# Optimization experiments

Measured on AMD Instinct MI355X. Metric: run time of the kernel, lower is better.

The kernel has to match this reference:

```python
import jax, jax.numpy as jnp
import numpy as np

B, S, D, H, HD = 4, 2048, 768, 12, 64
P = H * HD
LR = 0.1

def _ln(x, g, b, eps=1e-5):
    m = jnp.mean(x, axis=-1, keepdims=True)
    v = jnp.mean((x - m) ** 2, axis=-1, keepdims=True)
    return (x - m) / jnp.sqrt(v + eps) * g + b

def _modifier(x, w1, b1, w2, b2):
    # Linear -> GELU(exact) -> Linear, matching nn.Sequential(Linear, GELU, Linear)
    h = jax.nn.gelu(x @ w1.T + b1, approximate=False)
    return h @ w2.T + b2

def setup_inputs() -> dict:
    key = jax.random.key(0)
    ks = jax.random.split(key, 16)
    def n(k, shape, s=0.02):
        return jax.random.normal(k, shape, jnp.float32) * s
    inp = {}
    inp['x'] = jax.random.normal(ks[0], (B, S, D), jnp.float32)
    inp['ln_in_g'] = jnp.ones((D,), jnp.float32)
    inp['ln_in_b'] = jnp.zeros((D,), jnp.float32)
    inp['Wk'] = n(ks[1], (P, D))
    inp['Wv'] = n(ks[2], (P, D))
    inp['Wq'] = n(ks[3], (P, D))
    inp['km_w1'] = n(ks[4], (D // 4, D), 0.01); inp['km_b1'] = jnp.zeros((D // 4,), jnp.float32)
    inp['km_w2'] = n(ks[5], (P, D // 4), 0.01); inp['km_b2'] = jnp.zeros((P,), jnp.float32)
    inp['vm_w1'] = n(ks[6], (D // 4, D), 0.01); inp['vm_b1'] = jnp.zeros((D // 4,), jnp.float32)
    inp['vm_w2'] = n(ks[7], (P, D // 4), 0.01); inp['vm_b2'] = jnp.zeros((P,), jnp.float32)
    inp['qm_w1'] = n(ks[8], (D // 4, D), 0.01); inp['qm_b1'] = jnp.zeros((D // 4,), jnp.float32)
    inp['qm_w2'] = n(ks[9], (P, D // 4), 0.01); inp['qm_b2'] = jnp.zeros((P,), jnp.float32)
    inp['lnk_g'] = jnp.ones((HD,), jnp.float32); inp['lnk_b'] = jnp.zeros((HD,), jnp.float32)
    inp['lnv_g'] = jnp.ones((HD,), jnp.float32); inp['lnv_b'] = jnp.zeros((HD,), jnp.float32)
    inp['lnq_g'] = jnp.ones((HD,), jnp.float32); inp['lnq_b'] = jnp.zeros((HD,), jnp.float32)
    inp['Wo'] = n(ks[10], (D, P))
    inp['lr_scale'] = jnp.ones((H,), jnp.float32)
    inp['Wg'] = n(ks[11], (D, D))
    inp['bg'] = jnp.zeros((D,), jnp.float32)
    return inp

def reference(x, ln_in_g, ln_in_b, Wk, Wv, Wq,
              km_w1, km_b1, km_w2, km_b2,
              vm_w1, vm_b1, vm_w2, vm_b2,
              qm_w1, qm_b1, qm_w2, qm_b2,
              lnk_g, lnk_b, lnv_g, lnv_b, lnq_g, lnq_b,
              Wo, lr_scale, Wg, bg):
    b, s, d = x.shape
    xn = _ln(x, ln_in_g, ln_in_b)  # norm_input
    # data-dependent projections (context defaults to x_normed)
    k = xn @ Wk.T + 0.1 * _modifier(xn, km_w1, km_b1, km_w2, km_b2)
    v = xn @ Wv.T + 0.1 * _modifier(xn, vm_w1, vm_b1, vm_w2, vm_b2)
    q = xn @ Wq.T + 0.1 * _modifier(xn, qm_w1, qm_b1, qm_w2, qm_b2)
    k = _ln(k.reshape(b, s, H, HD), lnk_g, lnk_b)
    v = _ln(v.reshape(b, s, H, HD), lnv_g, lnv_b)
    q = _ln(q.reshape(b, s, H, HD), lnq_g, lnq_b)
    # scan over time: (s, b, h, d)
    k_s = jnp.transpose(k, (1, 0, 2, 3))
    v_s = jnp.transpose(v, (1, 0, 2, 3))
    q_s = jnp.transpose(q, (1, 0, 2, 3))
    lr = jax.nn.sigmoid(lr_scale) * LR * 2.0  # (H,)
    M0 = jnp.zeros((b, H, HD, HD), x.dtype)

    def step(M, kvq):
        k_t, v_t, q_t = kvq  # each (b, h, d)
        out_t = jnp.einsum('bhdk,bhk->bhd', M, q_t)  # read before update
        kn = k_t / (jnp.linalg.norm(k_t, axis=-1, keepdims=True) + 1e-6)
        pred = jnp.einsum('bhdk,bhk->bhd', M, kn)
        surprise = pred - v_t
        # M - outer(pred, kn) - lr * outer(surprise, kn), fused
        coef = pred + lr[None, :, None] * surprise  # (b, h, d)
        M_new = M - jnp.einsum('bhd,bhk->bhdk', coef, kn)
        return M_new, out_t

    M_final, outs = jax.lax.scan(step, M0, (k_s, v_s, q_s))  # outs: (s, b, h, d)
    out = jnp.transpose(outs, (1, 0, 2, 3)).reshape(b, s, H * HD)
    out = out @ Wo.T
    gate = jax.nn.sigmoid(x @ Wg.T + bg)  # output_gate on raw x
    out = gate * out
    return out, M_final
```

## Files before the change

### kernel.cpp

```cpp
#include <hip/hip_runtime.h>
#include <hip/hip_bf16.h>
#include <math.h>

#define B_ 4
#define S_ 2048
#define D_ 768
#define H_ 12
#define HD_ 64
#define P_ 768
#define M_ (B_*S_)
#define NCH 32
#define CH 64
#define BH (B_*H_)

typedef __hip_bfloat16 bf16;
typedef __attribute__((ext_vector_type(8))) short short8;
typedef __attribute__((ext_vector_type(4))) short s16x4;
typedef __attribute__((ext_vector_type(4))) float f32x4;

__device__ __forceinline__ float wave_reduce_sum(float v){
  #pragma unroll
  for (int off=32; off>0; off>>=1) v += __shfl_xor(v, off, 64);
  return v;
}
__device__ __forceinline__ float bf2f(bf16 h){ return __bfloat162float(h); }
__device__ __forceinline__ float us2f(unsigned short u){
  union{unsigned int i; float f;} z; z.i = ((unsigned int)u)<<16; return z.f;
}
__device__ __forceinline__ int adr(int row, int col){ return (row*128 + col*2) ^ ((row&7)<<4); }
__device__ __forceinline__ short8 lfrag(const char* base, int row, int col){
  return *(const short8*)(base + adr(row,col));
}
__device__ __forceinline__ short8 gfrag(const bf16* g, int row, int col){
  return *(const short8*)(g + row*64 + col);
}
__device__ __forceinline__ f32x4 MM(short8 a, short8 b, f32x4 c){
  return __builtin_amdgcn_mfma_f32_16x16x32_bf16(a, b, c, 0,0,0);
}
__device__ __forceinline__ short f2s(float v){ bf16 h = __float2bfloat16(v); return *(short*)&h; }
__device__ __forceinline__ void stpk(char* b, int n, int m0, float v0,float v1,float v2,float v3){
  s16x4 p = { f2s(v0), f2s(v1), f2s(v2), f2s(v3) };
  *(s16x4*)(b + adr(n, m0)) = p;
}
__device__ __forceinline__ void stpk_hl(char* bh, char* bl, int n, int m0,
                                        float v0,float v1,float v2,float v3){
  float h0=bf2f(__float2bfloat16(v0)), h1=bf2f(__float2bfloat16(v1));
  float h2=bf2f(__float2bfloat16(v2)), h3=bf2f(__float2bfloat16(v3));
  stpk(bh, n, m0, h0,h1,h2,h3);
  stpk(bl, n, m0, v0-h0, v1-h1, v2-h2, v3-h3);
}
__device__ __forceinline__ float4 ldpk2(const char* bh, const char* bl, int n, int m0){
  s16x4 a = *(const s16x4*)(bh + adr(n,m0));
  s16x4 b = *(const s16x4*)(bl + adr(n,m0));
  return make_float4(us2f((unsigned short)a[0])+us2f((unsigned short)b[0]),
                     us2f((unsigned short)a[1])+us2f((unsigned short)b[1]),
                     us2f((unsigned short)a[2])+us2f((unsigned short)b[2]),
                     us2f((unsigned short)a[3])+us2f((unsigned short)b[3]));
}
__device__ __forceinline__ void gl_lds(const bf16* g, const bf16* l){
  __builtin_amdgcn_global_load_lds(
      (const __attribute__((address_space(1))) void*)g,
      (__attribute__((address_space(3))) void*)l, 16, 0, 0);
}

__global__ __launch_bounds__(256) void pack_ln_kernel(
    const float* __restrict__ km1,const float* __restrict__ vm1,const float* __restrict__ qm1,
    const float* __restrict__ Wk,const float* __restrict__ Wv,const float* __restrict__ Wq,
    const float* __restrict__ k2,const float* __restrict__ v2,const float* __restrict__ q2,
    const float* __restrict__ Wo,const float* __restrict__ Wg,
    const float* __restrict__ kb1,const float* __restrict__ vb1,const float* __restrict__ qb1,
    const float* __restrict__ kb2,const float* __restrict__ vb2,const float* __restrict__ qb2,
    const float* __restrict__ lnkg,const float* __restrict__ lnvg,const float* __restrict__ lnqg,
    const float* __restrict__ lnkb,const float* __restrict__ lnvb,const float* __restrict__ lnqb,
    bf16* __restrict__ Whb, bf16* __restrict__ Wkvqb, bf16* __restrict__ Wob,
    bf16* __restrict__ Wgb, float* __restrict__ biasb,
    const float* __restrict__ x, const float* __restrict__ lng_in, const float* __restrict__ lnb_in,
    bf16* __restrict__ xn, bf16* __restrict__ xb)
{
  if (blockIdx.x >= 15181){
    int row = blockIdx.x - 15181;
    const float* xr = x + (size_t)row*D_;
    int t = threadIdx.x;
    float v0 = xr[t], v1 = xr[t+256], v2 = xr[t+512];
    float s  = v0+v1+v2;
    float sq = v0*v0+v1*v1+v2*v2;
    s = wave_reduce_sum(s); sq = wave_reduce_sum(sq);
    __shared__ float red[8];
    int w = t>>6;
    if ((t&63)==0){ red[w]=s; red[4+w]=sq; }
    __syncthreads();
    s  = red[0]+red[1]+red[2]+red[3];
    sq = red[4]+red[5]+red[6]+red[7];
    float mean = s*(1.f/D_);
    float var  = sq*(1.f/D_) - mean*mean;
    float inv  = rsqrtf(var + 1e-5f);
    bf16* xnr = xn + (size_t)row*D_;
    bf16* xbr = xb + (size_t)row*D_;
    xnr[t]     = __float2bfloat16((v0-mean)*inv*lng_in[t]     + lnb_in[t]);
    xnr[t+256] = __float2bfloat16((v1-mean)*inv*lng_in[t+256] + lnb_in[t+256]);
    xnr[t+512] = __float2bfloat16((v2-mean)*inv*lng_in[t+512] + lnb_in[t+512]);
    xbr[t] = __float2bfloat16(v0); xbr[t+256] = __float2bfloat16(v1); xbr[t+512] = __float2bfloat16(v2);
    return;
  }
  int i = blockIdx.x*256 + threadIdx.x;
  if (i < 491520){
    int r = i/768, c = i%768;
    float v = 0.f;
    if (r < 192) v = km1[r*768+c];
    else if (r < 384) v = vm1[(r-192)*768+c];
    else if (r < 576) v = qm1[(r-384)*768+c];
    Whb[i] = __float2bfloat16(v);
  } else if (i < 2703360){
    int i2 = i - 491520;
    int r = i2/960, c = i2%960;
    int p = r/768, rr = r%768;
    const float* W  = (p==0)?Wk:(p==1)?Wv:Wq;
    const float* w2 = (p==0)?k2:(p==1)?v2:q2;
    float v = (c < 768) ? W[(size_t)rr*768+c] : 0.1f*w2[(size_t)rr*192 + (c-768)];
    Wkvqb[i2] = __float2bfloat16(v);
  } else if (i < 3293184){
    int i2 = i - 2703360;
    Wob[i2] = __float2bfloat16(Wo[i2]);
  } else if (i < 3883008){
    int i2 = i - 3293184;
    Wgb[i2] = __float2bfloat16(Wg[i2]);
  } else if (i < 3886272){
    int i2 = i - 3883008;
    if (i2 < 576){
      biasb[i2] = (i2<192)? kb1[i2] : (i2<384)? vb1[i2-192] : qb1[i2-384];
    } else if (i2 < 2880){
      int r = i2-576; int p = r/768, rr = r%768;
      const float* b2 = (p==0)?kb2:(p==1)?vb2:qb2;
      biasb[i2] = 0.1f*b2[rr];
    } else if (i2 < 3072){
      int k3 = i2-2880; int gg=k3/64, cc=k3%64;
      biasb[i2] = (gg==0?lnkg:gg==1?lnvg:lnqg)[cc];
    } else {
      int k3 = i2-3072; int gg=k3/64, cc=k3%64;
      biasb[i2] = (gg==0?lnkb:gg==1?lnvb:lnqb)[cc];
    }
  }
}

template<int MODE>
__device__ __forceinline__ void gemm_core(
    const bf16* __restrict__ A1, int lda1, int K1,
    const bf16* __restrict__ A2, int lda2, int K2, int a2_gstride,
    const bf16* __restrict__ Bw, int ldb, int ngroup,
    const float* __restrict__ bias, const void* __restrict__ extra,
    const float* __restrict__ lng, const float* __restrict__ lnb,
    void* __restrict__ outp, int Nout,
    int bx, int by, int g, char* smemraw)
{
  bf16 (*Asm)[128*32] = (bf16 (*)[128*32])smemraw;
  bf16 (*Bsm)[128*32] = (bf16 (*)[128*32])(smemraw + 3*128*32*2);
  const int t = threadIdx.x;
  const int w = t>>6, L = t&63;
  const int m0 = bx*128, n0 = by*128;
  const int wm = w>>1, wn = w&1;
  const int Ktot = K1 + K2;
  const int nk = Ktot >> 5;

  const int srow = L>>2;
  const int scol8 = ((L&3) ^ ((L>>2)&3))*8;

  int aoff[4], boff[4];
  #pragma unroll
  for (int f=0;f<4;f++){
    int arow = wm*64 + f*16 + (L&15);
    int brow = wn*64 + f*16 + (L&15);
    aoff[f] = arow*32 + (((L>>4) ^ (arow&3))<<3);
    boff[f] = brow*32 + (((L>>4) ^ (brow&3))<<3);
  }

  const bf16* BrowBase = Bw + (size_t)(g*ngroup + n0)*ldb;

  auto STAGE = [&](int buf, int k0){
    const bf16* Ab; int lda; int acol;
    if (k0 < K1){ Ab = A1; lda = lda1; acol = k0 + scol8; }
    else        { Ab = A2; lda = lda2; acol = (k0-K1) + g*a2_gstride + scol8; }
    #pragma unroll
    for (int i=0;i<2;i++){
      int row = w*32 + i*16 + srow;
      gl_lds(Ab + (size_t)(m0+row)*lda + acol,         &Asm[buf][w*1024 + i*512]);
      gl_lds(BrowBase + (size_t)row*ldb + k0 + scol8,  &Bsm[buf][w*1024 + i*512]);
    }
  };

  f32x4 acc[4][4];
  #pragma unroll
  for (int i=0;i<4;i++)
    #pragma unroll
    for (int j=0;j<4;j++) acc[i][j] = (f32x4){0.f,0.f,0.f,0.f};

  STAGE(0, 0);
  STAGE(1, 32);
  int rd = 0;
  for (int kt=0; kt<nk; ++kt){
    if (kt == nk-1) asm volatile("s_waitcnt vmcnt(0)" ::: "memory");
    else            asm volatile("s_waitcnt vmcnt(4)" ::: "memory");
    asm volatile("s_waitcnt lgkmcnt(0)" ::: "memory");
    __builtin_amdgcn_s_barrier();
    __builtin_amdgcn_sched_barrier(0);
    if (kt+2 < nk){
      int st = rd+2; if (st>=3) st-=3;
      STAGE(st, (kt+2)<<5);
    }
    const bf16* As = Asm[rd];
    const bf16* Bs = Bsm[rd];
    short8 af[4], bfr[4];
    #pragma unroll
    for (int f=0;f<4;f++){
      af[f]  = *(const short8*)&As[aoff[f]];
      bfr[f] = *(const short8*)&Bs[boff[f]];
    }
    #pragma unroll
    for (int i=0;i<4;i++)
      #pragma unroll
      for (int j=0;j<4;j++)
        acc[i][j] = MM(af[i], bfr[j], acc[i][j]);
    rd = (rd==2)?0:rd+1;
  }

  if (MODE==1){
    float gco[4], bco[4];
    #pragma unroll
    for (int j=0;j<4;j++){ int cc = j*16 + (L&15); gco[j] = lng[g*64+cc]; bco[j] = lnb[g*64+cc]; }
    #pragma unroll
    for (int i=0;i<4;i++){
      #pragma unroll
      for (int r=0;r<4;r++){
        float v[4];
        #pragma unroll
        for (int j=0;j<4;j++){
          int n = n0 + wn*64 + j*16 + (L&15);
          v[j] = acc[i][j][r] + bias[g*768 + n];
        }
        float s1 = v[0]+v[1]+v[2]+v[3];
        float s2 = v[0]*v[0]+v[1]*v[1]+v[2]*v[2]+v[3]*v[3];
        #pragma unroll
        for (int mk=1; mk<16; mk<<=1){ s1 += __shfl_xor(s1, mk, 64); s2 += __shfl_xor(s2, mk, 64); }
        float mean = s1*(1.f/64.f);
        float var  = s2*(1.f/64.f) - mean*mean;
        float inv  = rsqrtf(var + 1e-5f);
        float y[4];
        #pragma unroll
        for (int j=0;j<4;j++) y[j] = (v[j]-mean)*inv*gco[j] + bco[j];
        if (g==0){
          float n2 = y[0]*y[0]+y[1]*y[1]+y[2]*y[2]+y[3]*y[3];
          #pragma unroll
          for (int mk=1; mk<16; mk<<=1) n2 += __shfl_xor(n2, mk, 64);
          float sc = 1.f/(sqrtf(n2)+1e-6f);
          #pragma unroll
          for (int j=0;j<4;j++) y[j] *= sc;
        }
        int m = m0 + wm*64 + i*16 + (L>>4)*4 + r;
        int b_ = m>>11, s_ = m&2047;
        #pragma unroll
        for (int j=0;j<4;j++){
          int n = n0 + wn*64 + j*16 + (L&15);
          int h_ = n>>6, hd = n&63;
          ((bf16*)outp)[((((size_t)g*B_ + b_)*H_ + h_)*S_ + s_)*HD_ + hd] = __float2bfloat16(y[j]);
        }
      }
    }
  } else {
    #pragma unroll
    for (int i=0;i<4;i++){
      #pragma unroll
      for (int j=0;j<4;j++){
        #pragma unroll
        for (int r=0;r<4;r++){
          int m = m0 + wm*64 + i*16 + (L>>4)*4 + r;
          int n = n0 + wn*64 + j*16 + (L&15);
          float val = acc[i][j][r];
          if (MODE==0){
            if (n < Nout){
              val += bias[n];
              float ge = 0.5f*val*(1.f + erff(val*0.70710678f));
              ((bf16*)outp)[(size_t)m*Nout + n] = __float2bfloat16(ge);
            }
          } else if (MODE==4){
            ((bf16*)outp)[(size_t)m*Nout + n] = __float2bfloat16(val);
          } else {
            float g2 = bf2f(((const bf16*)extra)[(size_t)m*768 + n]) + bias[n];
            float gate = 1.f/(1.f + __expf(-g2));
            ((float*)outp)[(size_t)m*Nout + n] = val * gate;
          }
        }
      }
    }
  }
}

template<int MODE>
__global__ __launch_bounds__(256) void gemm_kernel(
    const bf16* __restrict__ A1, int lda1, int K1,
    const bf16* __restrict__ A2, int lda2, int K2, int a2_gstride,
    const bf16* __restrict__ Bw, int ldb, int ngroup,
    const float* __restrict__ bias, const void* __restrict__ extra,
    const float* __restrict__ lng, const float* __restrict__ lnb,
    void* __restrict__ outp, int Nout)
{
  __shared__ __align__(16) char smem[49152];
  gemm_core<MODE>(A1, lda1, K1, A2, lda2, K2, a2_gstride, Bw, ldb, ngroup,
                  bias, extra, lng, lnb, outp, Nout,
                  blockIdx.x, blockIdx.y, blockIdx.z, smem);
}

__global__ __launch_bounds__(256) void prep_kernel(
    const bf16* __restrict__ kvqb, const float* __restrict__ lr_scale,
    bf16* __restrict__ WKng, bf16* __restrict__ WVTg,
    bf16* __restrict__ AcThi, bf16* __restrict__ AcTlo, bf16* __restrict__ Bcb)
{
  __shared__ __align__(16) char T1[8192];
  __shared__ __align__(16) char T2[8192];
  __shared__ __align__(16) char T3[8192];
  __shared__ __align__(16) char T4[8192];
  __shared__ __align__(16) char T5[8192];

  const int c = blockIdx.x, bh = blockIdx.y;
  const int h = bh % H_;
  const int t = threadIdx.x, w = t>>6, L = t&63;
  const size_t PS = (size_t)B_*H_*S_*HD_;
  const size_t base_k = (size_t)bh*S_*HD_ + (size_t)c*CH*HD_;
  const float lr = 0.2f/(1.f + __expf(-lr_scale[h]));
  const float beta = 1.f + lr;
  const size_t cb = ((size_t)bh*NCH + c)*4096;
  const bf16* Kg = kvqb + base_k;
  const bf16* Vg = kvqb + PS + base_k;

  const int fr = L&15, fc = (L>>4)*8;
  const int m0 = 16*w + (L>>4)*4;
  const int nb = L&15;

  {
    short8 aK[2];
    #pragma unroll
    for (int kk=0;kk<2;kk++) aK[kk] = gfrag(Kg, 16*w+fr, kk*32+fc);
    #pragma unroll
    for (int nt=0;nt<4;nt++){
      f32x4 g = (f32x4){0.f,0.f,0.f,0.f};
      #pragma unroll
      for (int kk=0;kk<2;kk++) g = MM(aK[kk], gfrag(Kg, 16*nt+fr, kk*32+fc), g);
      int n = 16*nt + nb;
      float pv[4], ptv[4], tv[4];
      #pragma unroll
      for (int r=0;r<4;r++){
        int m = m0 + r;
        float val = beta*g[r];
        pv[r]  = (n>m)? val : 0.f;
        ptv[r] = (m>n)? val : 0.f;
        tv[r]  = ((n==m)?1.f:0.f) - pv[r];
      }
      stpk(T3, n, m0, pv[0],pv[1],pv[2],pv[3]);
      stpk(T4, n, m0, ptv[0],ptv[1],ptv[2],ptv[3]);
      stpk_hl(T1, T2, n, m0, tv[0],tv[1],tv[2],tv[3]);
    }
  }
  __syncthreads();

  #pragma unroll
  for (int s=0; s<6; ++s){
    const bool do_upd = (s>=1), do_sq = (s<=4);
    f32x4 upd[4], c1[4], c2[4];
    float4 tr[4];
    short8 aPT[2];
    #pragma unroll
    for (int kk=0;kk<2;kk++) aPT[kk] = lfrag(T4, 16*w+fr, kk*32+fc);
    if (do_upd){
      short8 b1[4][2], b2[4][2];
      #pragma unroll
      for (int nt=0;nt<4;nt++){
        #pragma unroll
        for (int kk=0;kk<2;kk++){
          b1[nt][kk] = lfrag(T1, 16*nt+fr, kk*32+fc);
          b2[nt][kk] = lfrag(T2, 16*nt+fr, kk*32+fc);
        }
        upd[nt] = (f32x4){0.f,0.f,0.f,0.f};
      }
      #pragma unroll
      for (int nt=0;nt<4;nt++)
        #pragma unroll
        for (int kk=0;kk<2;kk++){
          upd[nt] = MM(aPT[kk], b1[nt][kk], upd[nt]);
          upd[nt] = MM(aPT[kk], b2[nt][kk], upd[nt]);
        }
      #pragma unroll
      for (int nt=0;nt<4;nt++) tr[nt] = ldpk2(T1, T2, 16*nt+nb, m0);
    }
    if (do_sq){
      short8 aP[2], bPT[4][2], bP[4][2];
      #pragma unroll
      for (int kk=0;kk<2;kk++) aP[kk] = lfrag(T3, 16*w+fr, kk*32+fc);
      #pragma unroll
      for (int nt=0;nt<4;nt++){
        #pragma unroll
        for (int kk=0;kk<2;kk++){
          bPT[nt][kk] = lfrag(T4, 16*nt+fr, kk*32+fc);
          bP[nt][kk]  = lfrag(T3, 16*nt+fr, kk*32+fc);
        }
        c1[nt] = (f32x4){0.f,0.f,0.f,0.f};
        c2[nt] = (f32x4){0.f,0.f,0.f,0.f};
      }
      #pragma unroll
      for (int nt=0;nt<4;nt++)
        #pragma unroll
        for (int kk=0;kk<2;kk++){
          c1[nt] = MM(aP[kk],  bPT[nt][kk], c1[nt]);
          c2[nt] = MM(aPT[kk], bP[nt][kk],  c2[nt]);
        }
    }
    __syncthreads();
    if (do_upd){
      #pragma unroll
      for (int nt=0;nt<4;nt++){
        int n = 16*nt + nb;
        stpk_hl(T1, T2, n, m0, tr[nt].x+upd[nt][0], tr[nt].y+upd[nt][1],
                               tr[nt].z+upd[nt][2], tr[nt].w+upd[nt][3]);
      }
    }
    if (do_sq){
      #pragma unroll
      for (int nt=0;nt<4;nt++){
        int n = 16*nt + nb;
        stpk(T4, n, m0, c1[nt][0],c1[nt][1],c1[nt][2],c1[nt][3]);
        stpk(T3, n, m0, c2[nt][0],c2[nt][1],c2[nt][2],c2[nt][3]);
      }
    }
    __syncthreads();
  }

  {
    short8 aKg[2], aVg[2];
    #pragma unroll
    for (int kk=0;kk<2;kk++){
      aKg[kk] = gfrag(Kg, 16*w+fr, kk*32+fc);
      aVg[kk] = gfrag(Vg, 16*w+fr, kk*32+fc);
    }
    #pragma unroll
    for (int nt=0;nt<4;nt++){
      f32x4 ck = (f32x4){0.f,0.f,0.f,0.f};
      f32x4 cv = (f32x4){0.f,0.f,0.f,0.f};
      int row = 16*nt + nb;
      #pragma unroll
      for (int kk=0;kk<2;kk++){
        short8 bi;
        int col0 = kk*32 + fc;
        #pragma unroll
        for (int e=0;e<8;e++) bi[e] = (col0+e == 16*nt+fr) ? (short)0x3F80 : (short)0;
        ck = MM(aKg[kk], bi, ck);
        cv = MM(aVg[kk], bi, cv);
      }
      stpk(T3, row, m0, ck[0],ck[1],ck[2],ck[3]);
      stpk(T4, row, m0, cv[0],cv[1],cv[2],cv[3]);
    }
  }
  __syncthreads();

  {
    short8 a1[2], a2[2];
    #pragma unroll
    for (int kk=0;kk<2;kk++){
      a1[kk] = lfrag(T1, 16*w+fr, kk*32+fc);
      a2[kk] = lfrag(T2, 16*w+fr, kk*32+fc);
    }
    f32x4 cwv[4], cwk[4];
    #pragma unroll
    for (int nt=0;nt<4;nt++){ cwv[nt]=(f32x4){0.f,0.f,0.f,0.f}; cwk[nt]=(f32x4){0.f,0.f,0.f,0.f}; }
    #pragma unroll
    for (int nt=0;nt<4;nt++)
      #pragma unroll
      for (int kk=0;kk<2;kk++){
        short8 bV = lfrag(T4, 16*nt+fr, kk*32+fc);
        cwv[nt] = MM(a1[kk], bV, cwv[nt]);
        cwv[nt] = MM(a2[kk], bV, cwv[nt]);
      }
    #pragma unroll
    for (int nt=0;nt<4;nt++)
      #pragma unroll
      for (int kk=0;kk<2;kk++){
        short8 bK = lfrag(T3, 16*nt+fr, kk*32+fc);
        cwk[nt] = MM(a1[kk], bK, cwk[nt]);
        cwk[nt] = MM(a2[kk], bK, cwk[nt]);
      }
    __syncthreads();
    #pragma unroll
    for (int nt=0;nt<4;nt++){
      int n = 16*nt + nb;
      stpk(T5, n, m0, cwv[nt][0],cwv[nt][1],cwv[nt][2],cwv[nt][3]);
      stpk(T4, n, m0, cwk[nt][0],cwk[nt][1],cwk[nt][2],cwk[nt][3]);
    }
  }
  __syncthreads();

  {
    int row = t>>2, seg = (t&3)*16;
    size_t go = cb + (size_t)row*64 + seg;
    *(short8*)(WVTg+go)   = *(const short8*)(T5 + adr(row,seg));
    *(short8*)(WVTg+go+8) = *(const short8*)(T5 + adr(row,seg+8));

    short8 aK2[2], aWKT[2];
    #pragma unroll
    for (int kk=0;kk<2;kk++){
      aK2[kk]  = lfrag(T3, 16*w+fr, kk*32+fc);
      aWKT[kk] = lfrag(T4, 16*w+fr, kk*32+fc);
    }
    f32x4 cBc[4], cWK[4], cAc[4];
    #pragma unroll
    for (int nt=0;nt<4;nt++){ cBc[nt]=(f32x4){0.f,0.f,0.f,0.f}; cWK[nt]=(f32x4){0.f,0.f,0.f,0.f}; cAc[nt]=(f32x4){0.f,0.f,0.f,0.f}; }
    #pragma unroll
    for (int nt=0;nt<4;nt++)
      #pragma unroll
      for (int kk=0;kk<2;kk++){
        short8 bWVT = lfrag(T5, 16*nt+fr, kk*32+fc);
        cBc[nt] = MM(aK2[kk], bWVT, cBc[nt]);
      }
    #pragma unroll
    for (int nt=0;nt<4;nt++)
      #pragma unroll
      for (int kk=0;kk<2;kk++){
        short8 b1 = lfrag(T1, 16*nt+fr, kk*32+fc);
        short8 b2 = lfrag(T2, 16*nt+fr, kk*32+fc);
        cWK[nt] = MM(aK2[kk], b1, cWK[nt]);
        cWK[nt] = MM(aK2[kk], b2, cWK[nt]);
      }
    #pragma unroll
    for (int nt=0;nt<4;nt++)
      #pragma unroll
      for (int kk=0;kk<2;kk++){
        short8 bK3 = lfrag(T3, 16*nt+fr, kk*32+fc);
        cAc[nt] = MM(aWKT[kk], bK3, cAc[nt]);
      }
    __syncthreads();
    #pragma unroll
    for (int nt=0;nt<4;nt++){
      int n = 16*nt + nb;
      stpk(T5, n, m0, lr*cBc[nt][0], lr*cBc[nt][1], lr*cBc[nt][2], lr*cBc[nt][3]);
      stpk(T3, n, m0, cWK[nt][0],cWK[nt][1],cWK[nt][2],cWK[nt][3]);
      float av[4];
      #pragma unroll
      for (int r=0;r<4;r++) av[r] = ((n==m0+r)?1.f:0.f) - beta*cAc[nt][r];
      stpk_hl(T1, T2, n, m0, av[0],av[1],av[2],av[3]);
    }
  }
  __syncthreads();

  {
    int row = t>>2, seg = (t&3)*16;
    size_t go = cb + (size_t)row*64 + seg;
    *(short8*)(AcThi+go)   = *(const short8*)(T1 + adr(row,seg));
    *(short8*)(AcThi+go+8) = *(const short8*)(T1 + adr(row,seg+8));
    *(short8*)(AcTlo+go)   = *(const short8*)(T2 + adr(row,seg));
    *(short8*)(AcTlo+go+8) = *(const short8*)(T2 + adr(row,seg+8));
    *(short8*)(Bcb+go)     = *(const short8*)(T5 + adr(row,seg));
    *(short8*)(Bcb+go+8)   = *(const short8*)(T5 + adr(row,seg+8));
    *(short8*)(WKng+go)    = *(const short8*)(T3 + adr(row,seg));
    *(short8*)(WKng+go+8)  = *(const short8*)(T3 + adr(row,seg+8));
  }
}

__global__ __launch_bounds__(256) void seq_kernel(
    const bf16* __restrict__ AcThi, const bf16* __restrict__ AcTlo,
    const bf16* __restrict__ Bcb,
    bf16* __restrict__ Mpref, bf16* __restrict__ Mplo, float* __restrict__ Mout,
    const bf16* __restrict__ xb, const bf16* __restrict__ Wgb, bf16* __restrict__ G2b)
{
  __shared__ __align__(16) char smem[49152];
  if (blockIdx.x >= BH){
    int bidx = blockIdx.x - BH;
    gemm_core<4>(xb, 768, 768, nullptr, 0, 0, 0, Wgb, 768, 768,
                 nullptr, nullptr, nullptr, nullptr, G2b, 768,
                 bidx & 63, bidx >> 6, 0, smem);
    return;
  }
  char* sH0 = smem;           char* sH1 = smem + 8192;
  char* sL0 = smem + 16384;   char* sL1 = smem + 24576;
  const int bh = blockIdx.x;
  const int t = threadIdx.x, w = t>>6, L = t&63;
  const size_t cbase = (size_t)bh*NCH*4096;
  const int fr = L&15, fc = (L>>4)*8;
  const int m0 = 16*w + (L>>4)*4;
  const int nb = L&15;

  { float4 z = {0.f,0.f,0.f,0.f};
    ((float4*)sH0)[t] = z; ((float4*)sH0)[t+256] = z;
    ((float4*)sL0)[t] = z; ((float4*)sL0)[t+256] = z;
    short8 zs = {0,0,0,0,0,0,0,0};
    ((short8*)(Mpref + cbase))[t] = zs; ((short8*)(Mpref + cbase))[t+256] = zs;
    ((short8*)(Mplo  + cbase))[t] = zs; ((short8*)(Mplo  + cbase))[t+256] = zs;
  }

  short8 Xh[2], Xl[2]; s16x4 Xc[4];
  short8 Yh[2], Yl[2]; s16x4 Yc[4];

  auto loadf = [&](short8 (&fh)[2], short8 (&fl)[2], s16x4 (&fbc)[4], int c){
    size_t cb = cbase + (size_t)c*4096;
    #pragma unroll
    for (int kk=0;kk<2;kk++){
      size_t o = cb + (size_t)(16*w + fr)*64 + kk*32 + fc;
      fh[kk] = *(const short8*)(AcThi + o);
      fl[kk] = *(const short8*)(AcTlo + o);
    }
    #pragma unroll
    for (int nt=0;nt<4;nt++)
      fbc[nt] = *(const s16x4*)(Bcb + cb + (size_t)(16*nt + nb)*64 + m0);
  };
  auto step = [&](short8 (&Ah)[2], short8 (&Al)[2], s16x4 (&Bc4)[4], int c,
                  char* rh, char* rl, char* wh, char* wl){
    __syncthreads();
    short8 bMh[4][2], bMl[4][2];
    #pragma unroll
    for (int nt=0;nt<4;nt++)
      #pragma unroll
      for (int kk=0;kk<2;kk++){
        bMh[nt][kk] = lfrag(rh, 16*nt+fr, kk*32+fc);
        bMl[nt][kk] = lfrag(rl, 16*nt+fr, kk*32+fc);
      }
    #pragma unroll
    for (int nt=0;nt<4;nt++){
      f32x4 acc = { us2f((unsigned short)Bc4[nt][0]), us2f((unsigned short)Bc4[nt][1]),
                    us2f((unsigned short)Bc4[nt][2]), us2f((unsigned short)Bc4[nt][3]) };
      acc = MM(Ah[0], bMh[nt][0], acc);
      acc = MM(Ah[1], bMh[nt][1], acc);
      acc = MM(Ah[0], bMl[nt][0], acc);
      acc = MM(Ah[1], bMl[nt][1], acc);
      acc = MM(Al[0], bMh[nt][0], acc);
      acc = MM(Al[1], bMh[nt][1], acc);
      int d = 16*nt + nb;
      float h[4], lo[4];
      #pragma unroll
      for (int r=0;r<4;r++){ h[r] = bf2f(__float2bfloat16(acc[r])); lo[r] = acc[r]-h[r]; }
      stpk(wh, d, m0, h[0],h[1],h[2],h[3]);
      stpk(wl, d, m0, lo[0],lo[1],lo[2],lo[3]);
      if (c < NCH-1){
        size_t go = cbase + (size_t)(c+1)*4096 + (size_t)d*64 + m0;
        s16x4 ph = { f2s(h[0]), f2s(h[1]), f2s(h[2]), f2s(h[3]) };
        s16x4 pl = { f2s(lo[0]), f2s(lo[1]), f2s(lo[2]), f2s(lo[3]) };
        *(s16x4*)(Mpref + go) = ph;
        *(s16x4*)(Mplo  + go) = pl;
      } else {
        float4 fv = { acc[0], acc[1], acc[2], acc[3] };
        *(float4*)(Mout + ((size_t)bh*64 + d)*64 + m0) = fv;
      }
    }
  };

  loadf(Xh,Xl,Xc,0);
  for (int c=0; c<NCH; c+=2){
    if (c+1 < NCH) loadf(Yh,Yl,Yc,c+1);
    step(Xh,Xl,Xc,c,   sH0,sL0, sH1,sL1);
    if (c+2 < NCH) loadf(Xh,Xl,Xc,c+2);
    step(Yh,Yl,Yc,c+1, sH1,sL1, sH0,sL0);
  }
}

__global__ __launch_bounds__(256) void outphase_kernel(
    const bf16* __restrict__ kvqb, const bf16* __restrict__ Mpref, const bf16* __restrict__ Mplo,
    const bf16* __restrict__ WKng, const bf16* __restrict__ WVTb,
    const float* __restrict__ lr_scale, bf16* __restrict__ attn)
{
  __shared__ __align__(16) char sUT[8192];
  __shared__ __align__(16) char sAT[8192];
  const int c = blockIdx.x, bh = blockIdx.y;
  const int b = bh / H_, h = bh % H_;
  const int t = threadIdx.x, w = t>>6, L = t&63;
  const size_t PS = (size_t)B_*H_*S_*HD_;
  const size_t cb = ((size_t)bh*NCH + c)*4096;
  const size_t base_k = (size_t)bh*S_*HD_ + (size_t)c*CH*HD_;
  const bf16* Kg = kvqb + base_k;
  const bf16* Qg = kvqb + 2*PS + base_k;
  const float lr = 0.2f/(1.f + __expf(-lr_scale[h]));
  const float beta = 1.f + lr;
  const int fr = L&15, fc = (L>>4)*8;
  const int m0 = 16*w + (L>>4)*4;
  const int nb = L&15;

  {
    short8 aKn[2];
    #pragma unroll
    for (int kk=0;kk<2;kk++) aKn[kk] = gfrag(Kg, 16*w+fr, kk*32+fc);
    #pragma unroll
    for (int nt=0;nt<4;nt++){
      f32x4 cat = (f32x4){0.f,0.f,0.f,0.f};
      #pragma unroll
      for (int kk=0;kk<2;kk++) cat = MM(aKn[kk], gfrag(Qg, 16*nt+fr, kk*32+fc), cat);
      int n = 16*nt + nb;
      float v[4];
      #pragma unroll
      for (int r=0;r<4;r++) v[r] = (m0+r < n)? cat[r] : 0.f;
      stpk(sAT, n, m0, v[0],v[1],v[2],v[3]);
    }
  }

  short8 mbh[4][2], mbl[4][2], qa[2], wa[2];
  #pragma unroll
  for (int kk=0;kk<2;kk++){
    qa[kk] = gfrag(Qg, 16*w+fr, kk*32+fc);
    wa[kk] = *(const short8*)(WKng + cb + (size_t)(16*w + fr)*64 + kk*32 + fc);
  }
  #pragma unroll
  for (int nt=0;nt<4;nt++)
    #pragma unroll
    for (int kk=0;kk<2;kk++){
      size_t o = cb + (size_t)(16*nt + fr)*64 + kk*32 + fc;
      mbh[nt][kk] = *(const short8*)(Mpref + o);
      mbl[nt][kk] = *(const short8*)(Mplo  + o);
    }
  f32x4 aout[4], ap[4];
  #pragma unroll
  for (int nt=0;nt<4;nt++){ aout[nt]=(f32x4){0.f,0.f,0.f,0.f}; ap[nt]=(f32x4){0.f,0.f,0.f,0.f}; }
  #pragma unroll
  for (int nt=0;nt<4;nt++)
    #pragma unroll
    for (int kk=0;kk<2;kk++){
      aout[nt] = MM(qa[kk], mbh[nt][kk], aout[nt]);
      aout[nt] = MM(qa[kk], mbl[nt][kk], aout[nt]);
      ap[nt]   = MM(wa[kk], mbh[nt][kk], ap[nt]);
      ap[nt]   = MM(wa[kk], mbl[nt][kk], ap[nt]);
    }
  #pragma unroll
  for (int nt=0;nt<4;nt++){
    s16x4 wv4 = *(const s16x4*)(WVTb + cb + (size_t)(nt*16 + (L&15))*64 + 16*w + (L>>4)*4);
    short us[4];
    #pragma unroll
    for (int r=0;r<4;r++){
      float wv = us2f((unsigned short)wv4[r]);
      us[r] = f2s(lr*wv - beta*ap[nt][r]);
    }
    int d = nt*16 + (L&15);
    int i0 = 16*w + (L>>4)*4;
    s16x4 pk = { us[0], us[1], us[2], us[3] };
    *(s16x4*)(sUT + adr(d, i0)) = pk;
  }
  __syncthreads();
  short8 ta[2], ub[4][2];
  #pragma unroll
  for (int kk=0;kk<2;kk++)
    ta[kk] = lfrag(sAT, 16*w+fr, kk*32+fc);
  #pragma unroll
  for (int nt=0;nt<4;nt++)
    #pragma unroll
    for (int kk=0;kk<2;kk++)
      ub[nt][kk] = lfrag(sUT, 16*nt + fr, kk*32 + fc);
  #pragma unroll
  for (int nt=0;nt<4;nt++)
    #pragma unroll
    for (int kk=0;kk<2;kk++)
      aout[nt] = MM(ta[kk], ub[nt][kk], aout[nt]);
  #pragma unroll
  for (int nt=0;nt<4;nt++)
    #pragma unroll
    for (int r=0;r<4;r++)
      attn[((size_t)b*S_ + (size_t)c*CH + 16*w + (L>>4)*4 + r)*P_ + h*HD_ + nt*16 + (L&15)]
        = __float2bfloat16(aout[nt][r]);
}

extern "C" void kernel_launch(void* const* d_in, const int* in_sizes, int n_in,
                              void* d_out, int out_size, void* d_ws, size_t ws_size,
                              hipStream_t stream)
{
  const float* x     = (const float*)d_in[0];
  const float* ln_g  = (const float*)d_in[1];
  const float* ln_b  = (const float*)d_in[2];
  const float* Wk    = (const float*)d_in[3];
  const float* Wv    = (const float*)d_in[4];
  const float* Wq    = (const float*)d_in[5];
  const float* km_w1 = (const float*)d_in[6];  const float* km_b1 = (const float*)d_in[7];
  const float* km_w2 = (const float*)d_in[8];  const float* km_b2 = (const float*)d_in[9];
  const float* vm_w1 = (const float*)d_in[10]; const float* vm_b1 = (const float*)d_in[11];
  const float* vm_w2 = (const float*)d_in[12]; const float* vm_b2 = (const float*)d_in[13];
  const float* qm_w1 = (const float*)d_in[14]; const float* qm_b1 = (const float*)d_in[15];
  const float* qm_w2 = (const float*)d_in[16]; const float* qm_b2 = (const float*)d_in[17];
  const float* lnk_g = (const float*)d_in[18]; const float* lnk_b = (const float*)d_in[19];
  const float* lnv_g = (const float*)d_in[20]; const float* lnv_b = (const float*)d_in[21];
  const float* lnq_g = (const float*)d_in[22]; const float* lnq_b = (const float*)d_in[23];
  const float* Wo    = (const float*)d_in[24];
  const float* lr_sc = (const float*)d_in[25];
  const float* Wg    = (const float*)d_in[26];
  const float* bg    = (const float*)d_in[27];

  const size_t CHB = (size_t)BH*NCH*4096;

  char* ws = (char*)d_ws;
  size_t o = 0;
  bf16* xnb   = (bf16*)(ws + o); o += (size_t)M_*D_*2;
  bf16* xb    = (bf16*)(ws + o); o += (size_t)M_*D_*2;
  bf16* Hb    = (bf16*)(ws + o); o += (size_t)M_*576*2;
  bf16* kvqb  = (bf16*)(ws + o); o += (size_t)3*M_*P_*2;
  bf16* attn  = (bf16*)(ws + o); o += (size_t)M_*P_*2;
  bf16* AcThi = (bf16*)(ws + o); o += CHB*2;
  bf16* AcTlo = (bf16*)(ws + o); o += CHB*2;
  bf16* Bcb   = (bf16*)(ws + o); o += CHB*2;
  bf16* WVTb  = (bf16*)(ws + o); o += CHB*2;
  bf16* WKng  = (bf16*)(ws + o); o += CHB*2;
  bf16* Mpref = (bf16*)(ws + o); o += CHB*2;
  bf16* Mplo  = (bf16*)(ws + o); o += CHB*2;
  bf16* Whb   = (bf16*)(ws + o); o += (size_t)640*768*2;
  bf16* Wkvqb = (bf16*)(ws + o); o += (size_t)2304*960*2;
  bf16* Wob   = (bf16*)(ws + o); o += (size_t)768*768*2;
  bf16* Wgb   = (bf16*)(ws + o); o += (size_t)768*768*2;
  float* biasb= (float*)(ws + o); o += 3264*4;
  bf16* G2b   = xnb;

  float* outF = (float*)d_out;
  float* Mout = outF + (size_t)M_*D_;

  pack_ln_kernel<<<15181 + M_, 256, 0, stream>>>(
      km_w1, vm_w1, qm_w1, Wk, Wv, Wq, km_w2, vm_w2, qm_w2, Wo, Wg,
      km_b1, vm_b1, qm_b1, km_b2, vm_b2, qm_b2,
      lnk_g, lnv_g, lnq_g, lnk_b, lnv_b, lnq_b,
      Whb, Wkvqb, Wob, Wgb, biasb,
      x, ln_g, ln_b, xnb, xb);

  gemm_kernel<0><<<dim3(64,5,1), 256, 0, stream>>>(xnb, 768, 768, nullptr, 0, 0, 0,
                                                   Whb, 768, 640, biasb, nullptr, nullptr, nullptr, Hb, 576);
  gemm_kernel<1><<<dim3(64,6,3), 256, 0, stream>>>(xnb, 768, 768, Hb, 576, 192, 192,
                                                   Wkvqb, 960, 768, biasb + 576, nullptr,
                                                   biasb + 2880, biasb + 3072, kvqb, 768);

  prep_kernel<<<dim3(NCH, BH), 256, 0, stream>>>(kvqb, lr_sc, WKng, WVTb, AcThi, AcTlo, Bcb);

  seq_kernel<<<BH + 384, 256, 0, stream>>>(AcThi, AcTlo, Bcb, Mpref, Mplo, Mout,
                                           xb, Wgb, G2b);

  outphase_kernel<<<dim3(NCH, BH), 256, 0, stream>>>(kvqb, Mpref, Mplo, WKng, WVTb, lr_sc, attn);

  gemm_kernel<3><<<dim3(64,6,1), 256, 0, stream>>>(attn, 768, 768, nullptr, 0, 0, 0,
                                                   Wob, 768, 768, bg, G2b, nullptr, nullptr, outF, 768);
}
```

Baseline: 245.4 us.

## Partition sequential state update by row-block per wave to remove block barriers

Changes the sequential chunk recurrence so each wave owns a 16-row slice of the 64x64 state, kept in a private LDS tile, and computes all four m-tiles for that slice. This removes the per-chunk __syncthreads and the double-buffered shared state, since each wave reads and writes only its own rows. In exchange each wave loads four times as many A fragments per chunk, which raises register pressure and global load traffic. Correctness relies on each row of the updated state depending only on that row of the previous state.

```diff
diff --git a/kernel.cpp b/kernel.cpp
--- a/kernel.cpp
+++ b/kernel.cpp
@@ -574,84 +574,80 @@
                  bidx & 63, bidx >> 6, 0, smem);
     return;
   }
-  char* sH0 = smem;           char* sH1 = smem + 8192;
-  char* sL0 = smem + 16384;   char* sL1 = smem + 24576;
   const int bh = blockIdx.x;
   const int t = threadIdx.x, w = t>>6, L = t&63;
   const size_t cbase = (size_t)bh*NCH*4096;
   const int fr = L&15, fc = (L>>4)*8;
-  const int m0 = 16*w + (L>>4)*4;
-  const int nb = L&15;
+  const int nb = L&15, cmr = (L>>4)*4;
+  char* th = smem + w*4096;
+  char* tl = th + 2048;
 
   { float4 z = {0.f,0.f,0.f,0.f};
-    ((float4*)sH0)[t] = z; ((float4*)sH0)[t+256] = z;
-    ((float4*)sL0)[t] = z; ((float4*)sL0)[t+256] = z;
+    ((float4*)th)[L] = z; ((float4*)th)[L+64] = z;
+    ((float4*)tl)[L] = z; ((float4*)tl)[L+64] = z;
     short8 zs = {0,0,0,0,0,0,0,0};
     ((short8*)(Mpref + cbase))[t] = zs; ((short8*)(Mpref + cbase))[t+256] = zs;
     ((short8*)(Mplo  + cbase))[t] = zs; ((short8*)(Mplo  + cbase))[t+256] = zs;
   }
 
-  short8 Xh[2], Xl[2]; s16x4 Xc[4];
-  short8 Yh[2], Yl[2]; s16x4 Yc[4];
-
-  auto loadf = [&](short8 (&fh)[2], short8 (&fl)[2], s16x4 (&fbc)[4], int c){
+  short8 XAh[4][2], XAl[4][2]; s16x4 XB[4];
+  short8 YAh[4][2], YAl[4][2]; s16x4 YB[4];
+
+  auto loadf = [&](short8 (&Ah)[4][2], short8 (&Al)[4][2], s16x4 (&Bc)[4], int c){
     size_t cb = cbase + (size_t)c*4096;
     #pragma unroll
+    for (int mt=0;mt<4;mt++){
+      #pragma unroll
+      for (int kk=0;kk<2;kk++){
+        size_t o = cb + (size_t)(16*mt + fr)*64 + kk*32 + fc;
+        Ah[mt][kk] = *(const short8*)(AcThi + o);
+        Al[mt][kk] = *(const short8*)(AcTlo + o);
+      }
+      Bc[mt] = *(const s16x4*)(Bcb + cb + (size_t)(16*w + nb)*64 + 16*mt + cmr);
+    }
+  };
+  auto step = [&](short8 (&Ah)[4][2], short8 (&Al)[4][2], s16x4 (&Bc)[4], int c){
+    short8 mh[2], ml[2];
+    #pragma unroll
     for (int kk=0;kk<2;kk++){
-      size_t o = cb + (size_t)(16*w + fr)*64 + kk*32 + fc;
-      fh[kk] = *(const short8*)(AcThi + o);
-      fl[kk] = *(const short8*)(AcTlo + o);
-    }
-    #pragma unroll
-    for (int nt=0;nt<4;nt++)
-      fbc[nt] = *(const s16x4*)(Bcb + cb + (size_t)(16*nt + nb)*64 + m0);
-  };
-  auto step = [&](short8 (&Ah)[2], short8 (&Al)[2], s16x4 (&Bc4)[4], int c,
-                  char* rh, char* rl, char* wh, char* wl){
-    __syncthreads();
-    short8 bMh[4][2], bMl[4][2];
-    #pragma unroll
-    for (int nt=0;nt<4;nt++)
-      #pragma unroll
-      for (int kk=0;kk<2;kk++){
-        bMh[nt][kk] = lfrag(rh, 16*nt+fr, kk*32+fc);
-        bMl[nt][kk] = lfrag(rl, 16*nt+fr, kk*32+fc);
-      }
-    #pragma unroll
-    for (int nt=0;nt<4;nt++){
-      f32x4 acc = { us2f((unsigned short)Bc4[nt][0]), us2f((unsigned short)Bc4[nt][1]),
-                    us2f((unsigned short)Bc4[nt][2]), us2f((unsigned short)Bc4[nt][3]) };
-      acc = MM(Ah[0], bMh[nt][0], acc);
-      acc = MM(Ah[1], bMh[nt][1], acc);
-      acc = MM(Ah[0], bMl[nt][0], acc);
-      acc = MM(Ah[1], bMl[nt][1], acc);
-      acc = MM(Al[0], bMh[nt][0], acc);
-      acc = MM(Al[1], bMh[nt][1], acc);
-      int d = 16*nt + nb;
+      mh[kk] = lfrag(th, fr, kk*32 + fc);
+      ml[kk] = lfrag(tl, fr, kk*32 + fc);
+    }
+    #pragma unroll
+    for (int mt=0;mt<4;mt++){
+      f32x4 acc = { us2f((unsigned short)Bc[mt][0]), us2f((unsigned short)Bc[mt][1]),
+                    us2f((unsigned short)Bc[mt][2]), us2f((unsigned short)Bc[mt][3]) };
+      acc = MM(Ah[mt][0], mh[0], acc);
+      acc = MM(Ah[mt][1], mh[1], acc);
+      acc = MM(Ah[mt][0], ml[0], acc);
+      acc = MM(Ah[mt][1], ml[1], acc);
+      acc = MM(Al[mt][0], mh[0], acc);
+      acc = MM(Al[mt][1], mh[1], acc);
+      int m0 = 16*mt + cmr;
       float h[4], lo[4];
       #pragma unroll
       for (int r=0;r<4;r++){ h[r] = bf2f(__float2bfloat16(acc[r])); lo[r] = acc[r]-h[r]; }
-      stpk(wh, d, m0, h[0],h[1],h[2],h[3]);
-      stpk(wl, d, m0, lo[0],lo[1],lo[2],lo[3]);
+      stpk(th, nb, m0, h[0],h[1],h[2],h[3]);
+      stpk(tl, nb, m0, lo[0],lo[1],lo[2],lo[3]);
       if (c < NCH-1){
-        size_t go = cbase + (size_t)(c+1)*4096 + (size_t)d*64 + m0;
+        size_t go = cbase + (size_t)(c+1)*4096 + (size_t)(16*w + nb)*64 + m0;
         s16x4 ph = { f2s(h[0]), f2s(h[1]), f2s(h[2]), f2s(h[3]) };
         s16x4 pl = { f2s(lo[0]), f2s(lo[1]), f2s(lo[2]), f2s(lo[3]) };
         *(s16x4*)(Mpref + go) = ph;
         *(s16x4*)(Mplo  + go) = pl;
       } else {
         float4 fv = { acc[0], acc[1], acc[2], acc[3] };
-        *(float4*)(Mout + ((size_t)bh*64 + d)*64 + m0) = fv;
+        *(float4*)(Mout + ((size_t)bh*64 + 16*w + nb)*64 + m0) = fv;
       }
     }
   };
 
-  loadf(Xh,Xl,Xc,0);
+  loadf(XAh,XAl,XB,0);
   for (int c=0; c<NCH; c+=2){
-    if (c+1 < NCH) loadf(Yh,Yl,Yc,c+1);
-    step(Xh,Xl,Xc,c,   sH0,sL0, sH1,sL1);
-    if (c+2 < NCH) loadf(Xh,Xl,Xc,c+2);
-    step(Yh,Yl,Yc,c+1, sH1,sL1, sH0,sL0);
+    if (c+1 < NCH) loadf(YAh,YAl,YB,c+1);
+    step(XAh,XAl,XB,c);
+    if (c+2 < NCH) loadf(XAh,XAl,XB,c+2);
+    step(YAh,YAl,YB,c+1);
   }
 }
 
```

New measurement: 271.5 us. 1.11x slower.

## Precompose chunk-pair transition matrices to halve the sequential chain length

Applied to the files above, without the earlier changes.

Adds a prep2 kernel that, for each pair of consecutive chunks, precomputes the composed transition A1*A0 and the combined offset term in hi/lo bf16 split form. The sequential kernel then advances the state two chunks per dependent step. It computes the odd-chunk state from the previous state in parallel with the even-chunk update rather than after it, roughly halving the serial dependency chain and the barriers. In exchange it adds a launch, extra workspace and global traffic, and some precision risk from composing the matrices in bf16 hi/lo form.

```diff
diff --git a/kernel.cpp b/kernel.cpp
--- a/kernel.cpp
+++ b/kernel.cpp
@@ -12,6 +12,7 @@
 #define NCH 32
 #define CH 64
 #define BH (B_*H_)
+#define NPAIR 16
 
 typedef __hip_bfloat16 bf16;
 typedef __attribute__((ext_vector_type(8))) short short8;
@@ -560,9 +561,100 @@
   }
 }
 
+__global__ __launch_bounds__(256) void prep2_kernel(
+    const bf16* __restrict__ AcThi, const bf16* __restrict__ AcTlo, const bf16* __restrict__ Bcb,
+    bf16* __restrict__ A2h, bf16* __restrict__ A2l,
+    bf16* __restrict__ BT2h, bf16* __restrict__ BT2l)
+{
+  __shared__ __align__(16) char TA[8192];
+  __shared__ __align__(16) char TB[8192];
+  const int i = blockIdx.x, bh = blockIdx.y;
+  const int t = threadIdx.x, w = t>>6, L = t&63;
+  const size_t cb0 = ((size_t)bh*NCH + 2*i)*4096;
+  const size_t cb1 = cb0 + 4096;
+  const size_t pb  = ((size_t)bh*NPAIR + i)*4096;
+  const int fr = L&15, fc = (L>>4)*8;
+  const int m0 = 16*w + (L>>4)*4;
+  const int nb = L&15;
+
+  {
+    short8 s0[2], s1[2];
+    #pragma unroll
+    for (int kk=0;kk<2;kk++){
+      s0[kk] = *(const short8*)(AcThi + cb0 + (size_t)(16*w+fr)*64 + kk*32 + fc);
+      s1[kk] = *(const short8*)(AcTlo + cb0 + (size_t)(16*w+fr)*64 + kk*32 + fc);
+    }
+    #pragma unroll
+    for (int nt=0;nt<4;nt++){
+      f32x4 c0v={0.f,0.f,0.f,0.f}, c1v={0.f,0.f,0.f,0.f};
+      #pragma unroll
+      for (int kk=0;kk<2;kk++){
+        short8 bi;
+        int col0 = kk*32 + fc;
+        #pragma unroll
+        for (int e=0;e<8;e++) bi[e] = (col0+e == 16*nt+fr) ? (short)0x3F80 : (short)0;
+        c0v = MM(s0[kk], bi, c0v);
+        c1v = MM(s1[kk], bi, c1v);
+      }
+      stpk(TA, 16*nt+nb, m0, c0v[0],c0v[1],c0v[2],c0v[3]);
+      stpk(TB, 16*nt+nb, m0, c1v[0],c1v[1],c1v[2],c1v[3]);
+    }
+  }
+  __syncthreads();
+  {
+    short8 aTh[2], aTl[2], gAh[2], gAl[2];
+    #pragma unroll
+    for (int kk=0;kk<2;kk++){
+      aTh[kk] = lfrag(TA, 16*w+fr, kk*32+fc);
+      aTl[kk] = lfrag(TB, 16*w+fr, kk*32+fc);
+      gAh[kk] = *(const short8*)(AcThi + cb1 + (size_t)(16*w+fr)*64 + kk*32 + fc);
+      gAl[kk] = *(const short8*)(AcTlo + cb1 + (size_t)(16*w+fr)*64 + kk*32 + fc);
+    }
+    #pragma unroll
+    for (int nt=0;nt<4;nt++){
+      short8 gBh[2], gBl[2], bB0[2];
+      #pragma unroll
+      for (int kk=0;kk<2;kk++){
+        gBh[kk] = *(const short8*)(AcThi + cb1 + (size_t)(16*nt+fr)*64 + kk*32 + fc);
+        gBl[kk] = *(const short8*)(AcTlo + cb1 + (size_t)(16*nt+fr)*64 + kk*32 + fc);
+        bB0[kk] = *(const short8*)(Bcb   + cb0 + (size_t)(16*nt+fr)*64 + kk*32 + fc);
+      }
+      f32x4 accA = {0.f,0.f,0.f,0.f};
+      s16x4 b1pk = *(const s16x4*)(Bcb + cb1 + (size_t)(16*nt+nb)*64 + m0);
+      f32x4 accB = { us2f((unsigned short)b1pk[0]), us2f((unsigned short)b1pk[1]),
+                     us2f((unsigned short)b1pk[2]), us2f((unsigned short)b1pk[3]) };
+      #pragma unroll
+      for (int kk=0;kk<2;kk++){
+        accA = MM(aTh[kk], gBh[kk], accA);
+        accA = MM(aTl[kk], gBh[kk], accA);
+        accA = MM(aTh[kk], gBl[kk], accA);
+        accB = MM(gAh[kk], bB0[kk], accB);
+        accB = MM(gAl[kk], bB0[kk], accB);
+      }
+      int n = 16*nt + nb;
+      size_t go = pb + (size_t)n*64 + m0;
+      float h0[4], l0[4], h1[4], l1[4];
+      #pragma unroll
+      for (int r=0;r<4;r++){
+        h0[r] = bf2f(__float2bfloat16(accA[r])); l0[r] = accA[r]-h0[r];
+        h1[r] = bf2f(__float2bfloat16(accB[r])); l1[r] = accB[r]-h1[r];
+      }
+      s16x4 pa = { f2s(h0[0]), f2s(h0[1]), f2s(h0[2]), f2s(h0[3]) };
+      s16x4 pbv= { f2s(l0[0]), f2s(l0[1]), f2s(l0[2]), f2s(l0[3]) };
+      s16x4 pc = { f2s(h1[0]), f2s(h1[1]), f2s(h1[2]), f2s(h1[3]) };
+      s16x4 pd = { f2s(l1[0]), f2s(l1[1]), f2s(l1[2]), f2s(l1[3]) };
+      *(s16x4*)(A2h  + go) = pa;
+      *(s16x4*)(A2l  + go) = pbv;
+      *(s16x4*)(BT2h + go) = pc;
+      *(s16x4*)(BT2l + go) = pd;
+    }
+  }
+}
+
 __global__ __launch_bounds__(256) void seq_kernel(
-    const bf16* __restrict__ AcThi, const bf16* __restrict__ AcTlo,
-    const bf16* __restrict__ Bcb,
+    const bf16* __restrict__ AcThi, const bf16* __restrict__ AcTlo, const bf16* __restrict__ Bcb,
+    const bf16* __restrict__ A2h, const bf16* __restrict__ A2l,
+    const bf16* __restrict__ BT2h, const bf16* __restrict__ BT2l,
     bf16* __restrict__ Mpref, bf16* __restrict__ Mplo, float* __restrict__ Mout,
     const bf16* __restrict__ xb, const bf16* __restrict__ Wgb, bf16* __restrict__ G2b)
 {
@@ -579,9 +671,10 @@
   const int bh = blockIdx.x;
   const int t = threadIdx.x, w = t>>6, L = t&63;
   const size_t cbase = (size_t)bh*NCH*4096;
+  const size_t pbase = (size_t)bh*NPAIR*4096;
   const int fr = L&15, fc = (L>>4)*8;
-  const int m0 = 16*w + (L>>4)*4;
-  const int nb = L&15;
+  const int nb = L&15, cmr = (L>>4)*4;
+  const int m0 = 16*w + cmr;
 
   { float4 z = {0.f,0.f,0.f,0.f};
     ((float4*)sH0)[t] = z; ((float4*)sH0)[t+256] = z;
@@ -591,67 +684,87 @@
     ((short8*)(Mplo  + cbase))[t] = zs; ((short8*)(Mplo  + cbase))[t+256] = zs;
   }
 
-  short8 Xh[2], Xl[2]; s16x4 Xc[4];
-  short8 Yh[2], Yl[2]; s16x4 Yc[4];
-
-  auto loadf = [&](short8 (&fh)[2], short8 (&fl)[2], s16x4 (&fbc)[4], int c){
-    size_t cb = cbase + (size_t)c*4096;
+  short8 A2hf[2], A2lf[2], Achf[2], Aclf[2];
+  auto loadA = [&](int i){
+    size_t pb  = pbase + (size_t)i*4096;
+    size_t cb0 = cbase + (size_t)(2*i)*4096;
     #pragma unroll
     for (int kk=0;kk<2;kk++){
-      size_t o = cb + (size_t)(16*w + fr)*64 + kk*32 + fc;
-      fh[kk] = *(const short8*)(AcThi + o);
-      fl[kk] = *(const short8*)(AcTlo + o);
-    }
-    #pragma unroll
-    for (int nt=0;nt<4;nt++)
-      fbc[nt] = *(const s16x4*)(Bcb + cb + (size_t)(16*nt + nb)*64 + m0);
+      size_t o = (size_t)(16*w+fr)*64 + kk*32 + fc;
+      A2hf[kk] = *(const short8*)(A2h + pb + o);
+      A2lf[kk] = *(const short8*)(A2l + pb + o);
+      Achf[kk] = *(const short8*)(AcThi + cb0 + o);
+      Aclf[kk] = *(const short8*)(AcTlo + cb0 + o);
+    }
   };
-  auto step = [&](short8 (&Ah)[2], short8 (&Al)[2], s16x4 (&Bc4)[4], int c,
-                  char* rh, char* rl, char* wh, char* wl){
+  loadA(0);
+  char *rh = sH0, *rl = sL0, *wh = sH1, *wl = sL1;
+
+  for (int i=0; i<NPAIR; ++i){
+    size_t pb  = pbase + (size_t)i*4096;
+    size_t cb0 = cbase + (size_t)(2*i)*4096;
     __syncthreads();
-    short8 bMh[4][2], bMl[4][2];
-    #pragma unroll
-    for (int nt=0;nt<4;nt++)
-      #pragma unroll
-      for (int kk=0;kk<2;kk++){
-        bMh[nt][kk] = lfrag(rh, 16*nt+fr, kk*32+fc);
-        bMl[nt][kk] = lfrag(rl, 16*nt+fr, kk*32+fc);
-      }
     #pragma unroll
     for (int nt=0;nt<4;nt++){
-      f32x4 acc = { us2f((unsigned short)Bc4[nt][0]), us2f((unsigned short)Bc4[nt][1]),
-                    us2f((unsigned short)Bc4[nt][2]), us2f((unsigned short)Bc4[nt][3]) };
-      acc = MM(Ah[0], bMh[nt][0], acc);
-      acc = MM(Ah[1], bMh[nt][1], acc);
-      acc = MM(Ah[0], bMl[nt][0], acc);
-      acc = MM(Ah[1], bMl[nt][1], acc);
-      acc = MM(Al[0], bMh[nt][0], acc);
-      acc = MM(Al[1], bMh[nt][1], acc);
+      short8 bMh[2], bMl[2];
+      #pragma unroll
+      for (int kk=0;kk<2;kk++){
+        bMh[kk] = lfrag(rh, 16*nt+fr, kk*32+fc);
+        bMl[kk] = lfrag(rl, 16*nt+fr, kk*32+fc);
+      }
+      f32x4 ae = {0.f,0.f,0.f,0.f}, ao = {0.f,0.f,0.f,0.f};
+      #pragma unroll
+      for (int kk=0;kk<2;kk++){
+        ae = MM(A2hf[kk], bMh[kk], ae);
+        ae = MM(A2hf[kk], bMl[kk], ae);
+        ae = MM(A2lf[kk], bMh[kk], ae);
+        ao = MM(Achf[kk], bMh[kk], ao);
+        ao = MM(Achf[kk], bMl[kk], ao);
+        ao = MM(Aclf[kk], bMh[kk], ao);
+      }
       int d = 16*nt + nb;
-      float h[4], lo[4];
-      #pragma unroll
-      for (int r=0;r<4;r++){ h[r] = bf2f(__float2bfloat16(acc[r])); lo[r] = acc[r]-h[r]; }
-      stpk(wh, d, m0, h[0],h[1],h[2],h[3]);
-      stpk(wl, d, m0, lo[0],lo[1],lo[2],lo[3]);
-      if (c < NCH-1){
-        size_t go = cbase + (size_t)(c+1)*4096 + (size_t)d*64 + m0;
+      size_t off = (size_t)d*64 + m0;
+      s16x4 b2h = *(const s16x4*)(BT2h + pb + off);
+      s16x4 b2l = *(const s16x4*)(BT2l + pb + off);
+      s16x4 b0  = *(const s16x4*)(Bcb  + cb0 + off);
+      float e[4], o[4];
+      #pragma unroll
+      for (int r=0;r<4;r++){
+        e[r] = ae[r] + us2f((unsigned short)b2h[r]) + us2f((unsigned short)b2l[r]);
+        o[r] = ao[r] + us2f((unsigned short)b0[r]);
+      }
+      {
+        float h[4], lo[4];
+        #pragma unroll
+        for (int r=0;r<4;r++){ h[r] = bf2f(__float2bfloat16(o[r])); lo[r] = o[r]-h[r]; }
+        size_t go = cbase + (size_t)(2*i+1)*4096 + off;
         s16x4 ph = { f2s(h[0]), f2s(h[1]), f2s(h[2]), f2s(h[3]) };
         s16x4 pl = { f2s(lo[0]), f2s(lo[1]), f2s(lo[2]), f2s(lo[3]) };
         *(s16x4*)(Mpref + go) = ph;
         *(s16x4*)(Mplo  + go) = pl;
-      } else {
-        float4 fv = { acc[0], acc[1], acc[2], acc[3] };
-        *(float4*)(Mout + ((size_t)bh*64 + d)*64 + m0) = fv;
-      }
-    }
-  };
-
-  loadf(Xh,Xl,Xc,0);
-  for (int c=0; c<NCH; c+=2){
-    if (c+1 < NCH) loadf(Yh,Yl,Yc,c+1);
-    step(Xh,Xl,Xc,c,   sH0,sL0, sH1,sL1);
-    if (c+2 < NCH) loadf(Xh,Xl,Xc,c+2);
-    step(Yh,Yl,Yc,c+1, sH1,sL1, sH0,sL0);
+      }
+      {
+        float h[4], lo[4];
+        #pragma unroll
+        for (int r=0;r<4;r++){ h[r] = bf2f(__float2bfloat16(e[r])); lo[r] = e[r]-h[r]; }
+        stpk(wh, d, m0, h[0],h[1],h[2],h[3]);
+        stpk(wl, d, m0, lo[0],lo[1],lo[2],lo[3]);
+        if (i < NPAIR-1){
+          size_t go = cbase + (size_t)(2*i+2)*4096 + off;
+          s16x4 ph = { f2s(h[0]), f2s(h[1]), f2s(h[2]), f2s(h[3]) };
+          s16x4 pl = { f2s(lo[0]), f2s(lo[1]), f2s(lo[2]), f2s(lo[3]) };
+          *(s16x4*)(Mpref + go) = ph;
+          *(s16x4*)(Mplo  + go) = pl;
+        } else {
+          float4 fv = { e[0], e[1], e[2], e[3] };
+          *(float4*)(Mout + ((size_t)bh*64 + d)*64 + m0) = fv;
+        }
+      }
+    }
+    if (i+1 < NPAIR) loadA(i+1);
+    char* tmp;
+    tmp = rh; rh = wh; wh = tmp;
+    tmp = rl; rl = wl; wl = tmp;
   }
 }
 
@@ -781,6 +894,7 @@
   const float* bg    = (const float*)d_in[27];
 
   const size_t CHB = (size_t)BH*NCH*4096;
+  const size_t PRB = (size_t)BH*NPAIR*4096;
 
   char* ws = (char*)d_ws;
   size_t o = 0;
@@ -796,6 +910,10 @@
   bf16* WKng  = (bf16*)(ws + o); o += CHB*2;
   bf16* Mpref = (bf16*)(ws + o); o += CHB*2;
   bf16* Mplo  = (bf16*)(ws + o); o += CHB*2;
+  bf16* A2h   = (bf16*)(ws + o); o += PRB*2;
+  bf16* A2l   = (bf16*)(ws + o); o += PRB*2;
+  bf16* BT2h  = (bf16*)(ws + o); o += PRB*2;
+  bf16* BT2l  = (bf16*)(ws + o); o += PRB*2;
   bf16* Whb   = (bf16*)(ws + o); o += (size_t)640*768*2;
   bf16* Wkvqb = (bf16*)(ws + o); o += (size_t)2304*960*2;
   bf16* Wob   = (bf16*)(ws + o); o += (size_t)768*768*2;
@@ -820,9 +938,10 @@
                                                    biasb + 2880, biasb + 3072, kvqb, 768);
 
   prep_kernel<<<dim3(NCH, BH), 256, 0, stream>>>(kvqb, lr_sc, WKng, WVTb, AcThi, AcTlo, Bcb);
-
-  seq_kernel<<<BH + 384, 256, 0, stream>>>(AcThi, AcTlo, Bcb, Mpref, Mplo, Mout,
-                                           xb, Wgb, G2b);
+  prep2_kernel<<<dim3(NPAIR, BH), 256, 0, stream>>>(AcThi, AcTlo, Bcb, A2h, A2l, BT2h, BT2l);
+
+  seq_kernel<<<BH + 384, 256, 0, stream>>>(AcThi, AcTlo, Bcb, A2h, A2l, BT2h, BT2l,
+                                           Mpref, Mplo, Mout, xb, Wgb, G2b);
 
   outphase_kernel<<<dim3(NCH, BH), 256, 0, stream>>>(kvqb, Mpref, Mplo, WKng, WVTb, lr_sc, attn);
 
```

New measurement: 269.3 us. +9.7%, slower.
